# Performance work log

Hardware: AMD Instinct MI355X
Metric: run time of the kernel (lower is better)

## Reference

```python
import jax, jax.numpy as jnp
import numpy as np

B, S, EMBED, HEADS = 2, 2048, 2048, 16
HEAD_DIM = EMBED // HEADS  # 128


def setup_inputs() -> dict:
    key = jax.random.key(0)
    k1, k2, k3 = jax.random.split(key, 3)
    x = jax.random.normal(k1, (B, S, EMBED), dtype=jnp.float32)
    # qkv_proj: Linear(EMBED -> 3*EMBED, bias=False); stored as [in, out]
    w_qkv = jax.random.normal(k2, (EMBED, 3 * EMBED), dtype=jnp.float32) / np.float32(np.sqrt(EMBED))
    # out_proj: Linear(EMBED -> EMBED, bias=False)
    w_out = jax.random.normal(k3, (EMBED, EMBED), dtype=jnp.float32) / np.float32(np.sqrt(EMBED))
    return {"x": x, "w_qkv": w_qkv, "w_out": w_out}


def reference(x, w_qkv, w_out):
    b, s, e = x.shape
    h, d = HEADS, e // HEADS
    qkv = x @ w_qkv                                  # [b, s, 3e]
    q, k, v = jnp.split(qkv, 3, axis=-1)             # each [b, s, e]
    q = q.reshape(b, s, h, d).transpose(0, 2, 1, 3)  # [b, h, s, d]
    k = k.reshape(b, s, h, d).transpose(0, 2, 1, 3)
    v = v.reshape(b, s, h, d).transpose(0, 2, 1, 3)
    scale = jnp.asarray(1.0 / np.sqrt(d), dtype=q.dtype)
    scores = jnp.einsum('bhqd,bhkd->bhqk', q, k) * scale  # [b, h, s, s]
    causal = jnp.tril(jnp.ones((s, s), dtype=bool))
    scores = jnp.where(causal, scores, -jnp.inf)
    attn = jax.nn.softmax(scores, axis=-1)
    ctx = jnp.einsum('bhqk,bhkd->bhqd', attn, v)     # [b, h, s, d]
    ctx = ctx.transpose(0, 2, 1, 3).reshape(b, s, e)
    return ctx @ w_out
```

## Files before the change

kernel.cpp:

```cpp
#include <hip/hip_runtime.h>
#include <cstdint>

#define S_LEN 2048
#define EMB   2048
#define NHEAD 16
#define HDIM  128
#define MROWS 4096
#define NQKV  6144

typedef __bf16 bf16x8 __attribute__((ext_vector_type(8)));
typedef __bf16 bf16x4 __attribute__((ext_vector_type(4)));
typedef float  f32x4  __attribute__((ext_vector_type(4)));

#define MFMA16(a, b, c) __builtin_amdgcn_mfma_f32_16x16x32_bf16((a), (b), (c), 0, 0, 0)

__device__ __forceinline__ unsigned short f2bf(float f) {
  unsigned u = __builtin_bit_cast(unsigned, f);
  u += 0x7fffu + ((u >> 16) & 1u);
  return (unsigned short)(u >> 16);
}
__device__ __forceinline__ float bf2f(unsigned short u) {
  unsigned v = ((unsigned)u) << 16;
  return __builtin_bit_cast(float, v);
}

__device__ __forceinline__ void gl_lds16(const unsigned short* g, unsigned short* l) {
  __builtin_amdgcn_global_load_lds(
      (const __attribute__((address_space(1))) void*)(uintptr_t)g,
      (__attribute__((address_space(3))) void*)(unsigned int)(uintptr_t)l,
      16, 0, 0);
}

__global__ void cast_bf16(const float* __restrict__ in, unsigned short* __restrict__ out, int n) {
  int i = (blockIdx.x * 256 + threadIdx.x) * 4;
  if (i >= n) return;
  float4 v = *(const float4*)(in + i);
  ushort4 o;
  o.x = f2bf(v.x); o.y = f2bf(v.y); o.z = f2bf(v.z); o.w = f2bf(v.w);
  *(ushort4*)(out + i) = o;
}

__global__ void transpose_cast(const float* __restrict__ in, unsigned short* __restrict__ out,
                               int R, int C) {
  __shared__ float tile[32][33];
  int bx = blockIdx.x << 5;
  int by = blockIdx.y << 5;
  int tx = threadIdx.x, ty = threadIdx.y;
  for (int j = 0; j < 32; j += 8)
    tile[ty + j][tx] = in[(size_t)(by + ty + j) * C + bx + tx];
  __syncthreads();
  for (int j = 0; j < 32; j += 8)
    out[(size_t)(bx + ty + j) * R + by + tx] = f2bf(tile[tx][ty + j]);
}

__device__ __forceinline__ void gemm_pipe(const unsigned short* __restrict__ Ap,
                                          const unsigned short* __restrict__ Bp,
                                          int m0, int n0, f32x4 (&acc)[4][4]) {
  extern __shared__ unsigned short lds[];
  unsigned short* As = lds;
  unsigned short* Bs = lds + 32768;
  const int tid = threadIdx.x;
  const int w = tid >> 6, lane = tid & 63;
  const int fr = lane & 15, g = lane >> 4;
  const int wm = (w >> 1) << 6;
  const int wn = (w & 1) << 6;
  const int q = tid >> 3, jp = tid & 7;

  auto stageA = [&](int buf, int kk) {
#pragma unroll
    for (int i = 0; i < 4; ++i) {
      const int row = q + (i << 6);
      gl_lds16(Ap + (size_t)(m0 + row) * 2048 + kk + ((jp ^ (row & 7)) << 3),
               As + buf * 16384 + (row << 6) + (jp << 3));
    }
  };
  auto stageB = [&](int buf, int kk) {
#pragma unroll
    for (int i = 0; i < 2; ++i) {
      const int row = q + (i << 6);
      gl_lds16(Bp + (size_t)(n0 + row) * 2048 + kk + ((jp ^ (row & 7)) << 3),
               Bs + buf * 8192 + (row << 6) + (jp << 3));
    }
  };

  stageA(0, 0); stageB(0, 0);
  int cur = 0;
#pragma unroll 2
  for (int t = 0; t < 32; ++t) {
    if (t < 31) {
      const int kn = (t + 1) << 6;
      stageA(cur ^ 1, kn); stageB(cur ^ 1, kn);
      asm volatile("s_waitcnt vmcnt(6)" ::: "memory");
    } else {
      asm volatile("s_waitcnt vmcnt(0)" ::: "memory");
    }
    __builtin_amdgcn_s_barrier();
    asm volatile("" ::: "memory");

    const unsigned short* Ab = As + cur * 16384;
    const unsigned short* Bb = Bs + cur * 8192;

    bf16x8 af[4][2], bv[2][2];
#pragma unroll
    for (int i = 0; i < 4; ++i)
#pragma unroll
      for (int ks = 0; ks < 2; ++ks)
        af[i][ks] = *(const bf16x8*)(Ab + ((wm + (i << 4) + fr) << 6) +
                                     ((((ks << 2) + g) ^ (fr & 7)) << 3));
#pragma unroll
    for (int j = 0; j < 2; ++j)
#pragma unroll
      for (int ks = 0; ks < 2; ++ks)
        bv[j][ks] = *(const bf16x8*)(Bb + ((wn + (j << 4) + fr) << 6) +
                                     ((((ks << 2) + g) ^ (fr & 7)) << 3));
    __builtin_amdgcn_s_setprio(1);
#pragma unroll
    for (int ks = 0; ks < 2; ++ks)
#pragma unroll
      for (int i = 0; i < 4; ++i)
#pragma unroll
        for (int j = 0; j < 2; ++j)
          acc[i][j] = MFMA16(af[i][ks], bv[j][ks], acc[i][j]);
    __builtin_amdgcn_s_setprio(0);
    asm volatile("" ::: "memory");
    __builtin_amdgcn_s_barrier();

    bf16x8 bw[2][2];
#pragma unroll
    for (int j = 0; j < 2; ++j)
#pragma unroll
      for (int ks = 0; ks < 2; ++ks)
        bw[j][ks] = *(const bf16x8*)(Bb + ((wn + ((j + 2) << 4) + fr) << 6) +
                                     ((((ks << 2) + g) ^ (fr & 7)) << 3));
    __builtin_amdgcn_s_setprio(1);
#pragma unroll
    for (int ks = 0; ks < 2; ++ks)
#pragma unroll
      for (int i = 0; i < 4; ++i)
#pragma unroll
        for (int j = 0; j < 2; ++j)
          acc[i][j + 2] = MFMA16(af[i][ks], bw[j][ks], acc[i][j + 2]);
    __builtin_amdgcn_s_setprio(0);
    asm volatile("" ::: "memory");
    __builtin_amdgcn_s_barrier();
    cur ^= 1;
  }
}

__global__ __launch_bounds__(512, 2) void gemm8_qkv(const unsigned short* __restrict__ A,
                                                    const unsigned short* __restrict__ Bt,
                                                    unsigned short* __restrict__ Qo,
                                                    unsigned short* __restrict__ Ko,
                                                    unsigned short* __restrict__ Vt) {
  const int bid = blockIdx.x;
  const int wg = (bid & 7) * 96 + (bid >> 3);
  const int mt = wg / 48, nt = wg - mt * 48;
  const int m0 = mt << 8, n0 = nt << 7;
  f32x4 acc[4][4] = {};
  gemm_pipe(A, Bt, m0, n0, acc);

  const int tid = threadIdx.x, w = tid >> 6, lane = tid & 63;
  const int fr = lane & 15, g = lane >> 4;
  const int wm = (w >> 1) << 6, wn = (w & 1) << 6;
  const int which = n0 >> 11;
  const int h = (n0 >> 7) & 15;
  const int bb = m0 >> 11;
  const int bh = bb * NHEAD + h;
  for (int i = 0; i < 4; ++i) {
    const int sl = (m0 & (S_LEN - 1)) + wm + (i << 4) + (g << 2);
    for (int j = 0; j < 4; ++j) {
      const int d = wn + (j << 4) + fr;
      if (which == 2) {
        ushort4 pk;
        pk.x = f2bf(acc[i][j][0]); pk.y = f2bf(acc[i][j][1]);
        pk.z = f2bf(acc[i][j][2]); pk.w = f2bf(acc[i][j][3]);
        *(ushort4*)(Vt + ((size_t)bh * HDIM + d) * S_LEN + sl) = pk;
      } else {
        unsigned short* dst = (which == 0) ? Qo : Ko;
        for (int r = 0; r < 4; ++r)
          dst[((size_t)bh * S_LEN + sl + r) * HDIM + d] = f2bf(acc[i][j][r]);
      }
    }
  }
}

__global__ __launch_bounds__(512, 2) void gemm8_out(const unsigned short* __restrict__ A,
                                                    const unsigned short* __restrict__ Bt,
                                                    float* __restrict__ C) {
  const int bid = blockIdx.x;
  const int wg = (bid & 7) * 32 + (bid >> 3);
  const int mt = wg >> 4, nt = wg & 15;
  const int m0 = mt << 8, n0 = nt << 7;
  f32x4 acc[4][4] = {};
  gemm_pipe(A, Bt, m0, n0, acc);

  const int tid = threadIdx.x, w = tid >> 6, lane = tid & 63;
  const int fr = lane & 15, g = lane >> 4;
  const int wm = (w >> 1) << 6, wn = (w & 1) << 6;
  for (int i = 0; i < 4; ++i) {
    const int row = m0 + wm + (i << 4) + (g << 2);
    for (int j = 0; j < 4; ++j) {
      const int col = n0 + wn + (j << 4) + fr;
      for (int r = 0; r < 4; ++r)
        C[(size_t)(row + r) * EMB + col] = acc[i][j][r];
    }
  }
}

__global__ __launch_bounds__(256, 3) void attn(const unsigned short* __restrict__ Qg,
                                               const unsigned short* __restrict__ Kg,
                                               const unsigned short* __restrict__ Vtg,
                                               unsigned short* __restrict__ ctx,
                                               unsigned short* __restrict__ Opart,
                                               float* __restrict__ Lp) {
  __shared__ __align__(16) unsigned short SA[16384];
  __shared__ __align__(16) unsigned short Ps[8192];
  unsigned short* Qs = SA;
  unsigned short* Ks = SA;
  unsigned short* Vs = SA + 8192;

  const int blk = blockIdx.x;
  const int bh = blk & 31;
  const int t = blk >> 5;
  int qt, kt0, nkt, part;
  if (t < 8)       { qt = t;     kt0 = 0;  nkt = 2 * t + 2;       part = -1; }
  else if (t < 16) { qt = t;     kt0 = 0;  nkt = 16;              part = (bh << 3) + (qt - 8); }
  else             { qt = t - 8; kt0 = 16; nkt = 2 * qt - 14;     part = 256 + (bh << 3) + (qt - 8); }

  const int tid = threadIdx.x, wave = tid >> 6, lane = tid & 63;
  const int fr = lane & 15, g = lane >> 4;

  const unsigned short* qsrc = Qg + ((size_t)bh * S_LEN + (qt << 7)) * HDIM;
  for (int i = 0; i < 8; ++i) {
    int s0 = (i * 256 + tid) << 3;
    int q = s0 >> 7, jp = (s0 >> 3) & 15;
    gl_lds16(qsrc + (q << 7) + ((jp ^ (q & 15)) << 3), Qs + s0);
  }
  __builtin_amdgcn_s_waitcnt(0);
  __syncthreads();

  bf16x8 qf[2][4];
  for (int nbq = 0; nbq < 2; ++nbq)
    for (int kd = 0; kd < 4; ++kd) {
      int q = (wave << 5) + (nbq << 4) + fr;
      qf[nbq][kd] = *(const bf16x8*)(Qs + (q << 7) + ((((kd << 2) + g) ^ fr) << 3));
    }
  __syncthreads();

  float lsum[2] = {0.f, 0.f};
  f32x4 oacc[2][8] = {};
  const float scale = 0.08838834764831845f;

  const unsigned short* kbase = Kg + (size_t)bh * S_LEN * HDIM;
  const unsigned short* vbase = Vtg + (size_t)bh * HDIM * S_LEN;

  for (int kti = 0; kti < nkt; ++kti) {
    const int kt = kt0 + kti;
    const unsigned short* ks = kbase + ((size_t)kt << 6) * HDIM;
    const unsigned short* vs = vbase + (kt << 6);
    for (int i = 0; i < 4; ++i) {
      int s0 = (i * 256 + tid) << 3;
      int key = s0 >> 7, jk = (s0 >> 3) & 15;
      gl_lds16(ks + (key << 7) + ((jk ^ (key & 15)) << 3), Ks + s0);
      int d = s0 >> 6, jv = (s0 >> 3) & 7;
      gl_lds16(vs + (size_t)d * S_LEN + ((jv ^ (d & 7)) << 3), Vs + s0);
    }
    __builtin_amdgcn_s_waitcnt(0);
    __syncthreads();

    f32x4 sacc[2][4] = {};
    for (int kd = 0; kd < 4; ++kd)
      for (int kb = 0; kb < 4; ++kb) {
        bf16x8 kf = *(const bf16x8*)(Ks + (((kb << 4) + fr) << 7) + ((((kd << 2) + g) ^ fr) << 3));
        sacc[0][kb] = MFMA16(kf, qf[0][kd], sacc[0][kb]);
        sacc[1][kb] = MFMA16(kf, qf[1][kd], sacc[1][kb]);
      }

    const bool diag = (kt >= 2 * qt);
    for (int nbq = 0; nbq < 2; ++nbq) {
      const int qg = (qt << 7) + (wave << 5) + (nbq << 4) + fr;
      float sum = 0.f;
      for (int kb = 0; kb < 4; ++kb) {
        float p[4];
        for (int r = 0; r < 4; ++r) {
          float v = sacc[nbq][kb][r] * scale;
          if (diag) {
            int keyg = (kt << 6) + (kb << 4) + (g << 2) + r;
            if (keyg > qg) v = -__builtin_inff();
          }
          p[r] = __expf(v);
          sum += p[r];
        }
        ushort4 pk;
        pk.x = f2bf(p[0]); pk.y = f2bf(p[1]); pk.z = f2bf(p[2]); pk.w = f2bf(p[3]);
        *(ushort4*)(Ps + (((wave << 3) + (nbq << 2) + kb) << 8) + (lane << 2)) = pk;
      }
      lsum[nbq] += sum;
    }

    __builtin_amdgcn_s_waitcnt(0);

    for (int kc = 0; kc < 2; ++kc) {
      const int kbr = (kc << 1) + (g >> 1);
      bf16x8 ap[2];
      for (int h2 = 0; h2 < 2; ++h2) {
        const unsigned short* pb =
            Ps + (((wave << 3) + (h2 << 2) + kbr) << 8) + ((g & 1) << 7) + (fr << 2);
        bf16x4 a0 = *(const bf16x4*)pb;
        bf16x4 a1 = *(const bf16x4*)(pb + 64);
        bf16x8 a;
        a[0] = a0[0]; a[1] = a0[1]; a[2] = a0[2]; a[3] = a0[3];
        a[4] = a1[0]; a[5] = a1[1]; a[6] = a1[2]; a[7] = a1[3];
        ap[h2] = a;
      }
      for (int nd = 0; nd < 8; ++nd) {
        bf16x8 bv = *(const bf16x8*)(Vs + (((nd << 4) + fr) << 6) + ((((kc << 2) + g) ^ (fr & 7)) << 3));
        oacc[0][nd] = MFMA16(ap[0], bv, oacc[0][nd]);
        oacc[1][nd] = MFMA16(ap[1], bv, oacc[1][nd]);
      }
    }
    __syncthreads();
  }

  for (int nbq = 0; nbq < 2; ++nbq) {
    lsum[nbq] += __shfl_xor(lsum[nbq], 16);
    lsum[nbq] += __shfl_xor(lsum[nbq], 32);
  }

  if (part < 0) {
    const int b = bh >> 4, h = bh & 15;
    for (int mq = 0; mq < 2; ++mq)
      for (int r = 0; r < 4; ++r) {
        float lv = __shfl(lsum[mq], (lane & 48) | ((g << 2) + r));
        const float il = 1.0f / lv;
        const int s = (qt << 7) + (wave << 5) + (mq << 4) + (g << 2) + r;
        unsigned short* dst = ctx + ((size_t)(b * S_LEN + s) * EMB) + (h << 7);
        for (int nd = 0; nd < 8; ++nd)
          dst[(nd << 4) + fr] = f2bf(oacc[mq][nd][r] * il);
      }
  } else {
    unsigned short* Ob = Opart + ((size_t)part << 14);
    for (int mq = 0; mq < 2; ++mq)
      for (int r = 0; r < 4; ++r) {
        const int ql = (wave << 5) + (mq << 4) + (g << 2) + r;
        unsigned short* dst = Ob + (ql << 7);
        for (int nd = 0; nd < 8; ++nd)
          dst[(nd << 4) + fr] = f2bf(oacc[mq][nd][r]);
      }
    if (g == 0)
      for (int nbq = 0; nbq < 2; ++nbq) {
        const int ql = (wave << 5) + (nbq << 4) + fr;
        Lp[(part << 7) + ql] = lsum[nbq];
      }
  }
}

__global__ void attn_combine(const unsigned short* __restrict__ Op,
                             const float* __restrict__ Lp,
                             unsigned short* __restrict__ ctx) {
  const int tid = threadIdx.x;
  const int rid = blockIdx.x * 16 + (tid >> 4);
  const int l16 = tid & 15;
  const int bh = rid >> 10;
  const int qtl = (rid >> 7) & 7;
  const int ql = rid & 127;
  const int p = (bh << 3) + qtl;
  const float lA = Lp[(p << 7) + ql];
  const float lB = Lp[((256 + p) << 7) + ql];
  const float il = 1.0f / (lA + lB);
  const int d0 = l16 << 3;
  const unsigned short* a = Op + ((size_t)p << 14) + (ql << 7) + d0;
  const unsigned short* b = Op + ((size_t)(256 + p) << 14) + (ql << 7) + d0;
  const int bb = bh >> 4, h = bh & 15;
  const int s = ((qtl + 8) << 7) + ql;
  unsigned short* dst = ctx + ((size_t)(bb * S_LEN + s) * EMB) + (h << 7) + d0;
  ushort4 va0 = *(const ushort4*)a, va1 = *(const ushort4*)(a + 4);
  ushort4 vb0 = *(const ushort4*)b, vb1 = *(const ushort4*)(b + 4);
  ushort4 o0, o1;
  o0.x = f2bf((bf2f(va0.x) + bf2f(vb0.x)) * il);
  o0.y = f2bf((bf2f(va0.y) + bf2f(vb0.y)) * il);
  o0.z = f2bf((bf2f(va0.z) + bf2f(vb0.z)) * il);
  o0.w = f2bf((bf2f(va0.w) + bf2f(vb0.w)) * il);
  o1.x = f2bf((bf2f(va1.x) + bf2f(vb1.x)) * il);
  o1.y = f2bf((bf2f(va1.y) + bf2f(vb1.y)) * il);
  o1.z = f2bf((bf2f(va1.z) + bf2f(vb1.z)) * il);
  o1.w = f2bf((bf2f(va1.w) + bf2f(vb1.w)) * il);
  *(ushort4*)dst = o0;
  *(ushort4*)(dst + 4) = o1;
}

extern "C" void kernel_launch(void* const* d_in, const int* in_sizes, int n_in,
                              void* d_out, int out_size, void* d_ws, size_t ws_size,
                              hipStream_t stream) {
  const float* x    = (const float*)d_in[0];
  const float* wqkv = (const float*)d_in[1];
  const float* wout = (const float*)d_in[2];
  float* out = (float*)d_out;

  unsigned short* ws = (unsigned short*)d_ws;
  const size_t NELEM = (size_t)MROWS * EMB;
  unsigned short* xb    = ws;
  unsigned short* wqkvT = xb + NELEM;
  unsigned short* woutT = wqkvT + (size_t)NQKV * EMB;
  unsigned short* Q     = woutT + (size_t)EMB * EMB;
  unsigned short* K     = Q + NELEM;
  unsigned short* Vt    = K + NELEM;
  unsigned short* ctx   = xb;
  unsigned short* Opart = wqkvT;
  float* Lp = (float*)(Opart + ((size_t)512 << 14));

  static bool attr_done = false;
  if (!attr_done) {
    (void)hipFuncSetAttribute((const void*)gemm8_qkv,
                              hipFuncAttributeMaxDynamicSharedMemorySize, 98304);
    (void)hipFuncSetAttribute((const void*)gemm8_out,
                              hipFuncAttributeMaxDynamicSharedMemorySize, 98304);
    attr_done = true;
  }

  cast_bf16<<<8192, 256, 0, stream>>>(x, xb, (int)NELEM);
  transpose_cast<<<dim3(NQKV / 32, EMB / 32), dim3(32, 8), 0, stream>>>(wqkv, wqkvT, EMB, NQKV);
  transpose_cast<<<dim3(EMB / 32, EMB / 32), dim3(32, 8), 0, stream>>>(wout, woutT, EMB, EMB);
  gemm8_qkv<<<768, 512, 98304, stream>>>(xb, wqkvT, Q, K, Vt);
  attn<<<768, 256, 0, stream>>>(Q, K, Vt, ctx, Opart, Lp);
  attn_combine<<<2048, 256, 0, stream>>>(Opart, Lp, ctx);
  gemm8_out<<<256, 512, 98304, stream>>>(ctx, woutT, out);
}
```

Baseline: 364.6 us.

## Double-buffer K/V tiles in attention and simplify QKV GEMM to 128x128 tiles

The attention kernel now stages the next K/V tile into a second LDS buffer while computing on the current one, using dynamic shared memory (80 KB) and partial vmcnt waits in place of full waits. Occupancy drops from 3 to 2 blocks per CU to make room. The QKV projection GEMM is replaced by a simpler single-buffered 128x128 tile kernel with 256 threads, which loses the previous software pipeline and blocking swizzle. The output GEMM is unchanged apart from being moved in the file.

```diff
diff --git a/kernel.cpp b/kernel.cpp
--- a/kernel.cpp
+++ b/kernel.cpp
@@ -30,6 +30,8 @@
       (__attribute__((address_space(3))) void*)(unsigned int)(uintptr_t)l,
       16, 0, 0);
 }
+
+#define FENCE() asm volatile("" ::: "memory")
 
 __global__ void cast_bf16(const float* __restrict__ in, unsigned short* __restrict__ out, int n) {
   int i = (blockIdx.x * 256 + threadIdx.x) * 4;
@@ -53,115 +55,42 @@
     out[(size_t)(bx + ty + j) * R + by + tx] = f2bf(tile[tx][ty + j]);
 }
 
-__device__ __forceinline__ void gemm_pipe(const unsigned short* __restrict__ Ap,
-                                          const unsigned short* __restrict__ Bp,
-                                          int m0, int n0, f32x4 (&acc)[4][4]) {
-  extern __shared__ unsigned short lds[];
-  unsigned short* As = lds;
-  unsigned short* Bs = lds + 32768;
+__global__ __launch_bounds__(256, 3) void gemm_qkv(const unsigned short* __restrict__ A,
+                                                   const unsigned short* __restrict__ Bt,
+                                                   unsigned short* __restrict__ Qo,
+                                                   unsigned short* __restrict__ Ko,
+                                                   unsigned short* __restrict__ Vt) {
+  __shared__ __align__(16) unsigned short As[128 * 64];
+  __shared__ __align__(16) unsigned short Bs[128 * 64];
   const int tid = threadIdx.x;
-  const int w = tid >> 6, lane = tid & 63;
+  const int n0 = blockIdx.x << 7;
+  const int m0 = blockIdx.y << 7;
+  const int wave = tid >> 6, lane = tid & 63;
+  const int wm = (wave & 1) << 6, wn = (wave >> 1) << 6;
   const int fr = lane & 15, g = lane >> 4;
-  const int wm = (w >> 1) << 6;
-  const int wn = (w & 1) << 6;
-  const int q = tid >> 3, jp = tid & 7;
-
-  auto stageA = [&](int buf, int kk) {
-#pragma unroll
+  const int q = tid >> 3;
+  const int jp = tid & 7;
+  f32x4 acc[4][4] = {};
+  for (int k0 = 0; k0 < 2048; k0 += 64) {
     for (int i = 0; i < 4; ++i) {
-      const int row = q + (i << 6);
-      gl_lds16(Ap + (size_t)(m0 + row) * 2048 + kk + ((jp ^ (row & 7)) << 3),
-               As + buf * 16384 + (row << 6) + (jp << 3));
-    }
-  };
-  auto stageB = [&](int buf, int kk) {
-#pragma unroll
-    for (int i = 0; i < 2; ++i) {
-      const int row = q + (i << 6);
-      gl_lds16(Bp + (size_t)(n0 + row) * 2048 + kk + ((jp ^ (row & 7)) << 3),
-               Bs + buf * 8192 + (row << 6) + (jp << 3));
-    }
-  };
-
-  stageA(0, 0); stageB(0, 0);
-  int cur = 0;
-#pragma unroll 2
-  for (int t = 0; t < 32; ++t) {
-    if (t < 31) {
-      const int kn = (t + 1) << 6;
-      stageA(cur ^ 1, kn); stageB(cur ^ 1, kn);
-      asm volatile("s_waitcnt vmcnt(6)" ::: "memory");
-    } else {
-      asm volatile("s_waitcnt vmcnt(0)" ::: "memory");
-    }
-    __builtin_amdgcn_s_barrier();
-    asm volatile("" ::: "memory");
-
-    const unsigned short* Ab = As + cur * 16384;
-    const unsigned short* Bb = Bs + cur * 8192;
-
-    bf16x8 af[4][2], bv[2][2];
-#pragma unroll
-    for (int i = 0; i < 4; ++i)
-#pragma unroll
-      for (int ks = 0; ks < 2; ++ks)
-        af[i][ks] = *(const bf16x8*)(Ab + ((wm + (i << 4) + fr) << 6) +
-                                     ((((ks << 2) + g) ^ (fr & 7)) << 3));
-#pragma unroll
-    for (int j = 0; j < 2; ++j)
-#pragma unroll
-      for (int ks = 0; ks < 2; ++ks)
-        bv[j][ks] = *(const bf16x8*)(Bb + ((wn + (j << 4) + fr) << 6) +
-                                     ((((ks << 2) + g) ^ (fr & 7)) << 3));
-    __builtin_amdgcn_s_setprio(1);
-#pragma unroll
-    for (int ks = 0; ks < 2; ++ks)
-#pragma unroll
+      const int row = q + (i << 5);
+      const int jsw = (jp ^ (row & 7)) << 3;
+      gl_lds16(A + (size_t)(m0 + row) * 2048 + k0 + jsw, As + (row << 6) + (jp << 3));
+      gl_lds16(Bt + (size_t)(n0 + row) * 2048 + k0 + jsw, Bs + (row << 6) + (jp << 3));
+    }
+    __builtin_amdgcn_s_waitcnt(0);
+    __syncthreads();
+    for (int ks = 0; ks < 2; ++ks) {
+      const int slot = (((ks << 2) + g) ^ (fr & 7)) << 3;
+      bf16x8 af[4], bfv[4];
+      for (int i = 0; i < 4; ++i) af[i]  = *(const bf16x8*)(As + ((wm + (i << 4) + fr) << 6) + slot);
+      for (int j = 0; j < 4; ++j) bfv[j] = *(const bf16x8*)(Bs + ((wn + (j << 4) + fr) << 6) + slot);
       for (int i = 0; i < 4; ++i)
-#pragma unroll
-        for (int j = 0; j < 2; ++j)
-          acc[i][j] = MFMA16(af[i][ks], bv[j][ks], acc[i][j]);
-    __builtin_amdgcn_s_setprio(0);
-    asm volatile("" ::: "memory");
-    __builtin_amdgcn_s_barrier();
-
-    bf16x8 bw[2][2];
-#pragma unroll
-    for (int j = 0; j < 2; ++j)
-#pragma unroll
-      for (int ks = 0; ks < 2; ++ks)
-        bw[j][ks] = *(const bf16x8*)(Bb + ((wn + ((j + 2) << 4) + fr) << 6) +
-                                     ((((ks << 2) + g) ^ (fr & 7)) << 3));
-    __builtin_amdgcn_s_setprio(1);
-#pragma unroll
-    for (int ks = 0; ks < 2; ++ks)
-#pragma unroll
-      for (int i = 0; i < 4; ++i)
-#pragma unroll
-        for (int j = 0; j < 2; ++j)
-          acc[i][j + 2] = MFMA16(af[i][ks], bw[j][ks], acc[i][j + 2]);
-    __builtin_amdgcn_s_setprio(0);
-    asm volatile("" ::: "memory");
-    __builtin_amdgcn_s_barrier();
-    cur ^= 1;
-  }
-}
-
-__global__ __launch_bounds__(512, 2) void gemm8_qkv(const unsigned short* __restrict__ A,
-                                                    const unsigned short* __restrict__ Bt,
-                                                    unsigned short* __restrict__ Qo,
-                                                    unsigned short* __restrict__ Ko,
-                                                    unsigned short* __restrict__ Vt) {
-  const int bid = blockIdx.x;
-  const int wg = (bid & 7) * 96 + (bid >> 3);
-  const int mt = wg / 48, nt = wg - mt * 48;
-  const int m0 = mt << 8, n0 = nt << 7;
-  f32x4 acc[4][4] = {};
-  gemm_pipe(A, Bt, m0, n0, acc);
-
-  const int tid = threadIdx.x, w = tid >> 6, lane = tid & 63;
-  const int fr = lane & 15, g = lane >> 4;
-  const int wm = (w >> 1) << 6, wn = (w & 1) << 6;
+        for (int j = 0; j < 4; ++j)
+          acc[i][j] = MFMA16(af[i], bfv[j], acc[i][j]);
+    }
+    __syncthreads();
+  }
   const int which = n0 >> 11;
   const int h = (n0 >> 7) & 15;
   const int bb = m0 >> 11;
@@ -184,40 +113,16 @@
   }
 }
 
-__global__ __launch_bounds__(512, 2) void gemm8_out(const unsigned short* __restrict__ A,
-                                                    const unsigned short* __restrict__ Bt,
-                                                    float* __restrict__ C) {
-  const int bid = blockIdx.x;
-  const int wg = (bid & 7) * 32 + (bid >> 3);
-  const int mt = wg >> 4, nt = wg & 15;
-  const int m0 = mt << 8, n0 = nt << 7;
-  f32x4 acc[4][4] = {};
-  gemm_pipe(A, Bt, m0, n0, acc);
-
-  const int tid = threadIdx.x, w = tid >> 6, lane = tid & 63;
-  const int fr = lane & 15, g = lane >> 4;
-  const int wm = (w >> 1) << 6, wn = (w & 1) << 6;
-  for (int i = 0; i < 4; ++i) {
-    const int row = m0 + wm + (i << 4) + (g << 2);
-    for (int j = 0; j < 4; ++j) {
-      const int col = n0 + wn + (j << 4) + fr;
-      for (int r = 0; r < 4; ++r)
-        C[(size_t)(row + r) * EMB + col] = acc[i][j][r];
-    }
-  }
-}
-
-__global__ __launch_bounds__(256, 3) void attn(const unsigned short* __restrict__ Qg,
+__global__ __launch_bounds__(256, 2) void attn(const unsigned short* __restrict__ Qg,
                                                const unsigned short* __restrict__ Kg,
                                                const unsigned short* __restrict__ Vtg,
                                                unsigned short* __restrict__ ctx,
                                                unsigned short* __restrict__ Opart,
                                                float* __restrict__ Lp) {
-  __shared__ __align__(16) unsigned short SA[16384];
-  __shared__ __align__(16) unsigned short Ps[8192];
-  unsigned short* Qs = SA;
-  unsigned short* Ks = SA;
-  unsigned short* Vs = SA + 8192;
+  extern __shared__ __align__(16) unsigned short lds[];
+  unsigned short* KV = lds;
+  unsigned short* Ps = lds + 32768;
+  unsigned short* Qs = lds;
 
   const int blk = blockIdx.x;
   const int bh = blk & 31;
@@ -254,24 +159,41 @@
   const unsigned short* kbase = Kg + (size_t)bh * S_LEN * HDIM;
   const unsigned short* vbase = Vtg + (size_t)bh * HDIM * S_LEN;
 
-  for (int kti = 0; kti < nkt; ++kti) {
-    const int kt = kt0 + kti;
+  auto stageKV = [&](int cur, int kt) {
     const unsigned short* ks = kbase + ((size_t)kt << 6) * HDIM;
     const unsigned short* vs = vbase + (kt << 6);
+    unsigned short* Kd = KV + (cur << 13);
+    unsigned short* Vd = KV + 16384 + (cur << 13);
+#pragma unroll
     for (int i = 0; i < 4; ++i) {
       int s0 = (i * 256 + tid) << 3;
       int key = s0 >> 7, jk = (s0 >> 3) & 15;
-      gl_lds16(ks + (key << 7) + ((jk ^ (key & 15)) << 3), Ks + s0);
+      gl_lds16(ks + (key << 7) + ((jk ^ (key & 15)) << 3), Kd + s0);
       int d = s0 >> 6, jv = (s0 >> 3) & 7;
-      gl_lds16(vs + (size_t)d * S_LEN + ((jv ^ (d & 7)) << 3), Vs + s0);
-    }
-    __builtin_amdgcn_s_waitcnt(0);
-    __syncthreads();
+      gl_lds16(vs + (size_t)d * S_LEN + ((jv ^ (d & 7)) << 3), Vd + s0);
+    }
+  };
+
+  stageKV(0, kt0);
+
+  for (int kti = 0; kti < nkt; ++kti) {
+    const int cur = kti & 1;
+    const int kt = kt0 + kti;
+    if (kti + 1 < nkt) {
+      stageKV(cur ^ 1, kt + 1);
+      asm volatile("s_waitcnt vmcnt(8)" ::: "memory");
+    } else {
+      asm volatile("s_waitcnt vmcnt(0)" ::: "memory");
+    }
+    FENCE(); __builtin_amdgcn_s_barrier(); FENCE();
+
+    const unsigned short* Kc = KV + (cur << 13);
+    const unsigned short* Vc = KV + 16384 + (cur << 13);
 
     f32x4 sacc[2][4] = {};
     for (int kd = 0; kd < 4; ++kd)
       for (int kb = 0; kb < 4; ++kb) {
-        bf16x8 kf = *(const bf16x8*)(Ks + (((kb << 4) + fr) << 7) + ((((kd << 2) + g) ^ fr) << 3));
+        bf16x8 kf = *(const bf16x8*)(Kc + (((kb << 4) + fr) << 7) + ((((kd << 2) + g) ^ fr) << 3));
         sacc[0][kb] = MFMA16(kf, qf[0][kd], sacc[0][kb]);
         sacc[1][kb] = MFMA16(kf, qf[1][kd], sacc[1][kb]);
       }
@@ -292,13 +214,15 @@
           sum += p[r];
         }
         ushort4 pk;
-        pk.x = f2bf(p[0]); pk.y = f2bf(p[1]); pk.z = f2bf(p[2]); pk.w = f2bf(p[3]);
+        pk.x = f2bf(p[0]); pk.y = f2bf(p[1]);
+        pk.z = f2bf(p[2]); pk.w = f2bf(p[3]);
         *(ushort4*)(Ps + (((wave << 3) + (nbq << 2) + kb) << 8) + (lane << 2)) = pk;
       }
       lsum[nbq] += sum;
     }
 
-    __builtin_amdgcn_s_waitcnt(0);
+    asm volatile("s_waitcnt lgkmcnt(0)" ::: "memory");
+    __builtin_amdgcn_sched_barrier(0);
 
     for (int kc = 0; kc < 2; ++kc) {
       const int kbr = (kc << 1) + (g >> 1);
@@ -314,12 +238,12 @@
         ap[h2] = a;
       }
       for (int nd = 0; nd < 8; ++nd) {
-        bf16x8 bv = *(const bf16x8*)(Vs + (((nd << 4) + fr) << 6) + ((((kc << 2) + g) ^ (fr & 7)) << 3));
+        bf16x8 bv = *(const bf16x8*)(Vc + (((nd << 4) + fr) << 6) + ((((kc << 2) + g) ^ (fr & 7)) << 3));
         oacc[0][nd] = MFMA16(ap[0], bv, oacc[0][nd]);
         oacc[1][nd] = MFMA16(ap[1], bv, oacc[1][nd]);
       }
     }
-    __syncthreads();
+    FENCE(); __builtin_amdgcn_s_barrier(); FENCE();
   }
 
   for (int nbq = 0; nbq < 2; ++nbq) {
@@ -389,6 +313,123 @@
   *(ushort4*)(dst + 4) = o1;
 }
 
+__device__ __forceinline__ void gemm_pipe(const unsigned short* __restrict__ Ap,
+                                          const unsigned short* __restrict__ Bp,
+                                          int m0, int n0, f32x4 (&acc)[4][4]) {
+  extern __shared__ unsigned short glds[];
+  unsigned short* As = glds;
+  unsigned short* Bs = glds + 32768;
+  const int tid = threadIdx.x;
+  const int w = tid >> 6, lane = tid & 63;
+  const int fr = lane & 15, g = lane >> 4;
+  const int wm = (w >> 1) << 6;
+  const int wn = (w & 1) << 6;
+  const int q = tid >> 3, jp = tid & 7;
+
+  auto stageA = [&](int buf, int kk) {
+#pragma unroll
+    for (int i = 0; i < 4; ++i) {
+      const int row = q + (i << 6);
+      gl_lds16(Ap + (size_t)(m0 + row) * 2048 + kk + ((jp ^ (row & 7)) << 3),
+               As + buf * 16384 + (row << 6) + (jp << 3));
+    }
+  };
+  auto stageB = [&](int buf, int kk) {
+#pragma unroll
+    for (int i = 0; i < 2; ++i) {
+      const int row = q + (i << 6);
+      gl_lds16(Bp + (size_t)(n0 + row) * 2048 + kk + ((jp ^ (row & 7)) << 3),
+               Bs + buf * 8192 + (row << 6) + (jp << 3));
+    }
+  };
+
+  stageA(0, 0); stageB(0, 0);
+  int cur = 0;
+#pragma unroll 2
+  for (int t = 0; t < 32; ++t) {
+    if (t < 31) {
+      const int kn = (t + 1) << 6;
+      stageA(cur ^ 1, kn); stageB(cur ^ 1, kn);
+      asm volatile("s_waitcnt vmcnt(6)" ::: "memory");
+    } else {
+      asm volatile("s_waitcnt vmcnt(0)" ::: "memory");
+    }
+    __builtin_amdgcn_s_barrier();
+    FENCE();
+
+    const unsigned short* Ab = As + cur * 16384;
+    const unsigned short* Bb = Bs + cur * 8192;
+
+    bf16x8 af[4][2], bv[2][2];
+#pragma unroll
+    for (int i = 0; i < 4; ++i)
+#pragma unroll
+      for (int ks = 0; ks < 2; ++ks)
+        af[i][ks] = *(const bf16x8*)(Ab + ((wm + (i << 4) + fr) << 6) +
+                                     ((((ks << 2) + g) ^ (fr & 7)) << 3));
+#pragma unroll
+    for (int j = 0; j < 2; ++j)
+#pragma unroll
+      for (int ks = 0; ks < 2; ++ks)
+        bv[j][ks] = *(const bf16x8*)(Bb + ((wn + (j << 4) + fr) << 6) +
+                                     ((((ks << 2) + g) ^ (fr & 7)) << 3));
+    __builtin_amdgcn_s_setprio(1);
+#pragma unroll
+    for (int ks = 0; ks < 2; ++ks)
+#pragma unroll
+      for (int i = 0; i < 4; ++i)
+#pragma unroll
+        for (int j = 0; j < 2; ++j)
+          acc[i][j] = MFMA16(af[i][ks], bv[j][ks], acc[i][j]);
+    __builtin_amdgcn_s_setprio(0);
+    FENCE();
+    __builtin_amdgcn_s_barrier();
+
+    bf16x8 bw[2][2];
+#pragma unroll
+    for (int j = 0; j < 2; ++j)
+#pragma unroll
+      for (int ks = 0; ks < 2; ++ks)
+        bw[j][ks] = *(const bf16x8*)(Bb + ((wn + ((j + 2) << 4) + fr) << 6) +
+                                     ((((ks << 2) + g) ^ (fr & 7)) << 3));
+    __builtin_amdgcn_s_setprio(1);
+#pragma unroll
+    for (int ks = 0; ks < 2; ++ks)
+#pragma unroll
+      for (int i = 0; i < 4; ++i)
+#pragma unroll
+        for (int j = 0; j < 2; ++j)
+          acc[i][j + 2] = MFMA16(af[i][ks], bw[j][ks], acc[i][j + 2]);
+    __builtin_amdgcn_s_setprio(0);
+    FENCE();
+    __builtin_amdgcn_s_barrier();
+    cur ^= 1;
+  }
+}
+
+__global__ __launch_bounds__(512, 2) void gemm8_out(const unsigned short* __restrict__ A,
+                                                    const unsigned short* __restrict__ Bt,
+                                                    float* __restrict__ C) {
+  const int bid = blockIdx.x;
+  const int wg = (bid & 7) * 32 + (bid >> 3);
+  const int mt = wg >> 4, nt = wg & 15;
+  const int m0 = mt << 8, n0 = nt << 7;
+  f32x4 acc[4][4] = {};
+  gemm_pipe(A, Bt, m0, n0, acc);
+
+  const int tid = threadIdx.x, w = tid >> 6, lane = tid & 63;
+  const int fr = lane & 15, g = lane >> 4;
+  const int wm = (w >> 1) << 6, wn = (w & 1) << 6;
+  for (int i = 0; i < 4; ++i) {
+    const int row = m0 + wm + (i << 4) + (g << 2);
+    for (int j = 0; j < 4; ++j) {
+      const int col = n0 + wn + (j << 4) + fr;
+      for (int r = 0; r < 4; ++r)
+        C[(size_t)(row + r) * EMB + col] = acc[i][j][r];
+    }
+  }
+}
+
 extern "C" void kernel_launch(void* const* d_in, const int* in_sizes, int n_in,
                               void* d_out, int out_size, void* d_ws, size_t ws_size,
                               hipStream_t stream) {
@@ -411,8 +452,8 @@
 
   static bool attr_done = false;
   if (!attr_done) {
-    (void)hipFuncSetAttribute((const void*)gemm8_qkv,
-                              hipFuncAttributeMaxDynamicSharedMemorySize, 98304);
+    (void)hipFuncSetAttribute((const void*)attn,
+                              hipFuncAttributeMaxDynamicSharedMemorySize, 81920);
     (void)hipFuncSetAttribute((const void*)gemm8_out,
                               hipFuncAttributeMaxDynamicSharedMemorySize, 98304);
     attr_done = true;
@@ -421,8 +462,8 @@
   cast_bf16<<<8192, 256, 0, stream>>>(x, xb, (int)NELEM);
   transpose_cast<<<dim3(NQKV / 32, EMB / 32), dim3(32, 8), 0, stream>>>(wqkv, wqkvT, EMB, NQKV);
   transpose_cast<<<dim3(EMB / 32, EMB / 32), dim3(32, 8), 0, stream>>>(wout, woutT, EMB, EMB);
-  gemm8_qkv<<<768, 512, 98304, stream>>>(xb, wqkvT, Q, K, Vt);
-  attn<<<768, 256, 0, stream>>>(Q, K, Vt, ctx, Opart, Lp);
+  gemm_qkv<<<dim3(NQKV / 128, MROWS / 128), 256, 0, stream>>>(xb, wqkvT, Q, K, Vt);
+  attn<<<768, 256, 81920, stream>>>(Q, K, Vt, ctx, Opart, Lp);
   attn_combine<<<2048, 256, 0, stream>>>(Opart, Lp, ctx);
   gemm8_out<<<256, 512, 98304, stream>>>(ctx, woutT, out);
 }
```

New measurement: 358.8 us. About the same (-1.6%).
